# Optimization experiments

Hardware: AMD Instinct MI355X
Metric: run time of the kernel (lower is better)

Reference implementation:

```python
import jax, jax.numpy as jnp
import numpy as np

B, S, NE, E, H = 4, 2048, 8, 1024, 16
DH = E // H


def setup_inputs() -> dict:
    key = jax.random.key(0)
    ks = jax.random.split(key, 10)
    s = 0.02
    return {
        "x": jax.random.normal(ks[0], (B, S, E), dtype=jnp.float32),
        "w1": jax.random.normal(ks[1], (NE, 4 * E, E), dtype=jnp.float32) * s,
        "b1": jnp.zeros((NE, 4 * E), dtype=jnp.float32),
        "w2": jax.random.normal(ks[2], (NE, E, 4 * E), dtype=jnp.float32) * s,
        "b2": jnp.zeros((NE, E), dtype=jnp.float32),
        "in_proj_w": jax.random.normal(ks[3], (3 * E, E), dtype=jnp.float32) * s,
        "in_proj_b": jnp.zeros((3 * E,), dtype=jnp.float32),
        "out_w": jax.random.normal(ks[4], (E, E), dtype=jnp.float32) * s,
        "out_b": jnp.zeros((E,), dtype=jnp.float32),
        "expert_id": 3,
    }


def reference(x, w1, b1, w2, b2, in_proj_w, in_proj_b, out_w, out_b, expert_id):
    # Per-expert FFN: [B,S,E] -> [B,S,NE,E]
    h = jax.nn.relu(jnp.einsum("bse,nfe->bsnf", x, w1) + b1)
    eo = jnp.einsum("bsnf,nef->bsne", h, w2) + b2  # [B,S,NE,E]

    # Multihead self-attention over the expert axis, batched over (B,S).
    wq, wk, wv = in_proj_w[:E], in_proj_w[E:2 * E], in_proj_w[2 * E:]
    bq, bk, bv = in_proj_b[:E], in_proj_b[E:2 * E], in_proj_b[2 * E:]
    q = (eo @ wq.T + bq).reshape(B, S, NE, H, DH)
    k = (eo @ wk.T + bk).reshape(B, S, NE, H, DH)
    v = (eo @ wv.T + bv).reshape(B, S, NE, H, DH)

    scale = 1.0 / jnp.sqrt(jnp.asarray(DH, dtype=q.dtype))
    # torch additive float mask: tril of ONES added to logits (not -inf masking)
    add_mask = jnp.tril(jnp.ones((NE, NE), dtype=q.dtype))
    logits = jnp.einsum("bsqhd,bskhd->bshqk", q, k) * scale + add_mask
    attn = jax.nn.softmax(logits, axis=-1)
    o = jnp.einsum("bshqk,bskhd->bsqhd", attn, v).reshape(B, S, NE, E)
    o = o @ out_w.T + out_b  # [B,S,NE,E]

    return o[:, :, expert_id, :]  # [B,S,E]
```

## Files before the change

### kernel.cpp

```cpp
#include <hip/hip_runtime.h>

typedef __bf16 bf16x8 __attribute__((ext_vector_type(8)));
typedef float  f32x4  __attribute__((ext_vector_type(4)));

__device__ __forceinline__ float bf2f(unsigned short u) {
    union { unsigned int i; float f; } x; x.i = ((unsigned int)u) << 16; return x.f;
}
__device__ __forceinline__ unsigned short f2bf(float f) {
    union { float f; unsigned int i; } x; x.f = f;
    unsigned int r = x.i + 0x7fff + ((x.i >> 16) & 1);
    return (unsigned short)(r >> 16);
}

__device__ __forceinline__ void gload16(const void* g, void* l) {
    __builtin_amdgcn_global_load_lds(
        (const __attribute__((address_space(1))) void*)g,
        (__attribute__((address_space(3))) void*)l, 16, 0, 0);
}

__global__ __launch_bounds__(256) void cvt_f32_bf16(
    const float4* __restrict__ in, ushort4* __restrict__ out, long n4)
{
    long i = (long)blockIdx.x * blockDim.x + threadIdx.x;
    const long stride = (long)gridDim.x * blockDim.x;
    for (; i < n4; i += stride) {
        const float4 v = in[i];
        ushort4 o = { f2bf(v.x), f2bf(v.y), f2bf(v.z), f2bf(v.w) };
        out[i] = o;
    }
}

template<bool RELU, typename CT, bool QKV>
__global__ __launch_bounds__(512, 2) void gemm256(
    const ushort* __restrict__ A, long lda, long sAz,
    const ushort* __restrict__ B, long ldb, long sBz,
    const float* __restrict__ bias, long sBiasz,
    CT* __restrict__ C, long ldc, long sCz,
    ushort* __restrict__ qc, ushort* __restrict__ kvc,
    int K, const int* __restrict__ eid_p)
{
    const long z  = blockIdx.z;
    const int gx  = gridDim.x;
    const int nwg = gx * gridDim.y;
    int wg = blockIdx.y * gx + blockIdx.x;
    if ((nwg & 7) == 0) wg = (wg & 7) * (nwg >> 3) + (wg >> 3);
    const long n0 = (long)(wg % gx) * 256;
    const long m0 = (long)(wg / gx) * 256;

    if constexpr (QKV) {
        if (n0 < 1024 && z != (long)(*eid_p)) return;
    }
    A    += z * sAz;
    B    += z * sBz;
    bias += z * sBiasz;
    if constexpr (!QKV) C += z * sCz;

    __shared__ alignas(16) ushort As[4][256 * 32];
    __shared__ alignas(16) ushort Bs[4][256 * 32];

    const int t    = threadIdx.x;
    const int wid  = t >> 6;
    const int lane = t & 63;
    const int lr   = lane & 15;
    const int lq   = lane >> 4;
    const int wr   = wid >> 2;
    const int wc   = wid & 3;

    const int d0 = wid * 1024 + lane * 16;
    const int s0 = d0 ^ (((d0 >> 7) & 3) << 4);
    const int r0 = s0 >> 6;
    const int c0 = (s0 & 63) >> 1;
    const ushort* aG0 = A + (m0 + r0) * lda + c0;
    const ushort* aG1 = A + (m0 + r0 + 128) * lda + c0;
    const ushort* bG0 = B + (n0 + r0) * ldb + c0;
    const ushort* bG1 = B + (n0 + r0 + 128) * ldb + c0;
    const int ldsOff = wid * 512;

    const int chnk  = lq ^ ((lr >> 1) & 3);
    const int aBase = (wr * 128 + lr) * 32 + chnk * 8;
    const int bBase = (wc * 64  + lr) * 32 + chnk * 8;

    const int nt = K >> 5;

    #define STAGE(buf_, kt_) { \
        const long ko_ = (long)(kt_) * 32; \
        gload16(aG0 + ko_, (void*)&As[buf_][ldsOff]); \
        gload16(aG1 + ko_, (void*)&As[buf_][4096 + ldsOff]); \
        gload16(bG0 + ko_, (void*)&Bs[buf_][ldsOff]); \
        gload16(bG1 + ko_, (void*)&Bs[buf_][4096 + ldsOff]); }

    STAGE(0, 0)
    if (nt > 1) STAGE(1, 1)
    if (nt > 2) STAGE(2, 2)

    f32x4 acc[8][4];
#pragma unroll
    for (int i = 0; i < 8; i++)
#pragma unroll
        for (int j = 0; j < 4; j++) acc[i][j] = (f32x4){0.f, 0.f, 0.f, 0.f};

    for (int kt = 0; kt < nt; ++kt) {
        const int rem = nt - 1 - kt;
        if (rem >= 2)      asm volatile("s_waitcnt vmcnt(8)" ::: "memory");
        else if (rem == 1) asm volatile("s_waitcnt vmcnt(4)" ::: "memory");
        else               asm volatile("s_waitcnt vmcnt(0)" ::: "memory");
        __builtin_amdgcn_s_barrier();
        __builtin_amdgcn_sched_barrier(0);

        if (kt + 3 < nt) STAGE((kt + 3) & 3, kt + 3)

        const ushort* as_ = As[kt & 3];
        const ushort* bs_ = Bs[kt & 3];
        bf16x8 af[8], bfr[4];
#pragma unroll
        for (int i = 0; i < 8; i++) af[i]  = *(const bf16x8*)&as_[aBase + i * 512];
#pragma unroll
        for (int j = 0; j < 4; j++) bfr[j] = *(const bf16x8*)&bs_[bBase + j * 512];

        __builtin_amdgcn_s_setprio(1);
#pragma unroll
        for (int i = 0; i < 8; i++)
#pragma unroll
            for (int j = 0; j < 4; j++)
                acc[i][j] = __builtin_amdgcn_mfma_f32_16x16x32_bf16(af[i], bfr[j], acc[i][j], 0, 0, 0);
        __builtin_amdgcn_s_setprio(0);
    }
    #undef STAGE

#pragma unroll
    for (int j = 0; j < 4; j++) {
        const long col = n0 + wc * 64 + j * 16 + lr;
        const float bv = bias[col];
#pragma unroll
        for (int i = 0; i < 8; i++) {
            const long rbase = m0 + wr * 128 + i * 16 + lq * 4;
#pragma unroll
            for (int r = 0; r < 4; r++) {
                float v = acc[i][j][r] + bv;
                if (RELU) v = fmaxf(v, 0.f);
                const long row = rbase + r;
                if constexpr (QKV) {
                    if (col < 1024) qc[row * 1024 + col] = f2bf(v);
                    else            kvc[row * 16384 + z * 2048 + (col - 1024)] = f2bf(v);
                } else if constexpr (__is_same(CT, ushort)) {
                    C[row * ldc + col] = f2bf(v);
                } else {
                    C[row * ldc + col] = v;
                }
            }
        }
    }
}

__global__ __launch_bounds__(256) void attn_kernel(
    const ushort* __restrict__ qc, const ushort* __restrict__ kvc,
    const int* __restrict__ eid_p, ushort* __restrict__ o3)
{
    const size_t m = blockIdx.x;
    const int t    = threadIdx.x;
    const int h    = t >> 4;
    const int d0   = (t & 15) * 4;
    const int eid  = *eid_p;

    const ushort4 qu = *(const ushort4*)(qc + m * 1024 + h * 64 + d0);
    const float qv[4] = { bf2f(qu.x), bf2f(qu.y), bf2f(qu.z), bf2f(qu.w) };

    float l[8];
#pragma unroll
    for (int n = 0; n < 8; n++) {
        const ushort4 ku = *(const ushort4*)(kvc + (m * 8 + n) * 2048 + h * 64 + d0);
        float p = qv[0] * bf2f(ku.x) + qv[1] * bf2f(ku.y) + qv[2] * bf2f(ku.z) + qv[3] * bf2f(ku.w);
        p += __shfl_xor(p, 1);
        p += __shfl_xor(p, 2);
        p += __shfl_xor(p, 4);
        p += __shfl_xor(p, 8);
        l[n] = p * 0.125f + ((n <= eid) ? 1.0f : 0.0f);
    }
    float mx = l[0];
#pragma unroll
    for (int n = 1; n < 8; n++) mx = fmaxf(mx, l[n]);
    float e[8], s = 0.f;
#pragma unroll
    for (int n = 0; n < 8; n++) { e[n] = __expf(l[n] - mx); s += e[n]; }
    const float inv = 1.f / s;

    float o[4] = {0.f, 0.f, 0.f, 0.f};
#pragma unroll
    for (int n = 0; n < 8; n++) {
        const ushort4 vu = *(const ushort4*)(kvc + (m * 8 + n) * 2048 + 1024 + h * 64 + d0);
        const float a = e[n] * inv;
        o[0] += a * bf2f(vu.x); o[1] += a * bf2f(vu.y);
        o[2] += a * bf2f(vu.z); o[3] += a * bf2f(vu.w);
    }
    ushort4 ou = { f2bf(o[0]), f2bf(o[1]), f2bf(o[2]), f2bf(o[3]) };
    *(ushort4*)(o3 + m * 1024 + h * 64 + d0) = ou;
}

extern "C" void kernel_launch(void* const* d_in, const int* in_sizes, int n_in,
                              void* d_out, int out_size, void* d_ws, size_t ws_size,
                              hipStream_t stream)
{
    const float* x   = (const float*)d_in[0];
    const float* w1  = (const float*)d_in[1];
    const float* b1  = (const float*)d_in[2];
    const float* w2  = (const float*)d_in[3];
    const float* b2  = (const float*)d_in[4];
    const float* ipw = (const float*)d_in[5];
    const float* ipb = (const float*)d_in[6];
    const float* ow  = (const float*)d_in[7];
    const float* ob  = (const float*)d_in[8];
    const int*   eid = (const int*)d_in[9];

    char* ws = (char*)d_ws;
    size_t off = 0;
    auto alloc = [&](size_t bytes) { char* p = ws + off; off += (bytes + 255) & ~(size_t)255; return p; };
    ushort* w1b  = (ushort*)alloc(8LL * 4096 * 1024 * 2);
    ushort* w2b  = (ushort*)alloc(8LL * 1024 * 4096 * 2);
    ushort* ipwb = (ushort*)alloc(3LL * 1024 * 1024 * 2);
    ushort* owb  = (ushort*)alloc(1LL * 1024 * 1024 * 2);
    ushort* xb   = (ushort*)alloc(8192LL * 1024 * 2);
    ushort* o3b  = (ushort*)alloc(8192LL * 1024 * 2);
    const size_t fixed = off;

    long Mc = 2048;
    while (Mc > 256 && fixed + (size_t)Mc * 116736 + 2048 > ws_size) Mc >>= 1;
    ushort* hb  = (ushort*)alloc((size_t)Mc * 8 * 4096 * 2);
    ushort* eob = (ushort*)alloc((size_t)Mc * 8 * 1024 * 2);
    ushort* kvc = (ushort*)alloc((size_t)Mc * 8 * 2048 * 2);
    ushort* qc  = (ushort*)alloc((size_t)Mc * 1024 * 2);

    const dim3 blk(256);
    const dim3 blk5(512);
    const dim3 cgrid(2048);

    cvt_f32_bf16<<<cgrid, blk, 0, stream>>>((const float4*)w1,  (ushort4*)w1b,  8LL * 4096 * 1024 / 4);
    cvt_f32_bf16<<<cgrid, blk, 0, stream>>>((const float4*)w2,  (ushort4*)w2b,  8LL * 1024 * 4096 / 4);
    cvt_f32_bf16<<<cgrid, blk, 0, stream>>>((const float4*)ipw, (ushort4*)ipwb, 3LL * 1024 * 1024 / 4);
    cvt_f32_bf16<<<cgrid, blk, 0, stream>>>((const float4*)ow,  (ushort4*)owb,  1LL * 1024 * 1024 / 4);
    cvt_f32_bf16<<<cgrid, blk, 0, stream>>>((const float4*)x,   (ushort4*)xb,   8192LL * 1024 / 4);

    for (long m0 = 0; m0 < 8192; m0 += Mc) {
        const unsigned my = (unsigned)(Mc / 256);
        gemm256<true, ushort, false><<<dim3(16, my, 8), blk5, 0, stream>>>(
            xb + m0 * 1024, 1024, 0,
            w1b, 1024, 4096LL * 1024,
            b1, 4096,
            hb, 4096, (long)Mc * 4096,
            nullptr, nullptr, 1024, eid);
        gemm256<false, ushort, false><<<dim3(4, my, 8), blk5, 0, stream>>>(
            hb, 4096, (long)Mc * 4096,
            w2b, 4096, 1024LL * 4096,
            b2, 1024,
            eob, 1024, (long)Mc * 1024,
            nullptr, nullptr, 4096, eid);
        gemm256<false, ushort, true><<<dim3(12, my, 8), blk5, 0, stream>>>(
            eob, 1024, (long)Mc * 1024,
            ipwb, 1024, 0,
            ipb, 0,
            (ushort*)nullptr, 0, 0,
            qc, kvc, 1024, eid);
        attn_kernel<<<dim3((unsigned)Mc), blk, 0, stream>>>(
            qc, kvc, eid, o3b + m0 * 1024);
    }

    gemm256<false, float, false><<<dim3(4, 32, 1), blk5, 0, stream>>>(
        o3b, 1024, 0,
        owb, 1024, 0,
        ob, 0,
        (float*)d_out, 1024, 0,
        nullptr, nullptr, 1024, eid);
}
```

Before: 2.641 ms.

## Split GEMM k-loop into two barrier-separated MFMA phases with staggered A/B prefetch

Restructures the bf16 GEMM main loop so each k-tile is processed in two halves of four row fragments each. The global-to-LDS prefetch for A is issued in the first half and for B in the second, with barriers and waitcnts placed around each MFMA burst. The aim is to spread memory issue across the compute phases, interleave LDS reads with MFMA, and cut register use by holding four A fragments instead of eight. The cost is more barriers per iteration and reliance on hand-tuned vmcnt counts.

```diff
diff --git a/kernel.cpp b/kernel.cpp
--- a/kernel.cpp
+++ b/kernel.cpp
@@ -82,16 +82,18 @@
 
     const int nt = K >> 5;
 
-    #define STAGE(buf_, kt_) { \
-        const long ko_ = (long)(kt_) * 32; \
+    #define STAGE_A(buf_, kt_) { const long ko_ = (long)(kt_) * 32; \
         gload16(aG0 + ko_, (void*)&As[buf_][ldsOff]); \
-        gload16(aG1 + ko_, (void*)&As[buf_][4096 + ldsOff]); \
+        gload16(aG1 + ko_, (void*)&As[buf_][4096 + ldsOff]); }
+    #define STAGE_B(buf_, kt_) { const long ko_ = (long)(kt_) * 32; \
         gload16(bG0 + ko_, (void*)&Bs[buf_][ldsOff]); \
         gload16(bG1 + ko_, (void*)&Bs[buf_][4096 + ldsOff]); }
 
-    STAGE(0, 0)
-    if (nt > 1) STAGE(1, 1)
-    if (nt > 2) STAGE(2, 2)
+    STAGE_A(0, 0) STAGE_B(0, 0)
+    if (nt > 1) { STAGE_A(1, 1) STAGE_B(1, 1) }
+    if (nt > 2) { STAGE_A(2, 2) STAGE_B(2, 2) }
+    asm volatile("s_waitcnt vmcnt(8)" ::: "memory");
+    __builtin_amdgcn_s_barrier();
 
     f32x4 acc[8][4];
 #pragma unroll
@@ -100,32 +102,53 @@
         for (int j = 0; j < 4; j++) acc[i][j] = (f32x4){0.f, 0.f, 0.f, 0.f};
 
     for (int kt = 0; kt < nt; ++kt) {
-        const int rem = nt - 1 - kt;
-        if (rem >= 2)      asm volatile("s_waitcnt vmcnt(8)" ::: "memory");
-        else if (rem == 1) asm volatile("s_waitcnt vmcnt(4)" ::: "memory");
-        else               asm volatile("s_waitcnt vmcnt(0)" ::: "memory");
-        __builtin_amdgcn_s_barrier();
-        __builtin_amdgcn_sched_barrier(0);
-
-        if (kt + 3 < nt) STAGE((kt + 3) & 3, kt + 3)
-
-        const ushort* as_ = As[kt & 3];
-        const ushort* bs_ = Bs[kt & 3];
-        bf16x8 af[8], bfr[4];
-#pragma unroll
-        for (int i = 0; i < 8; i++) af[i]  = *(const bf16x8*)&as_[aBase + i * 512];
+        const int r = kt & 3;
+        const ushort* as_ = As[r];
+        const ushort* bs_ = Bs[r];
+        const bool pf = (kt + 3 < nt);
+
+        bf16x8 af[4], bfr[4];
+#pragma unroll
+        for (int i = 0; i < 4; i++) af[i]  = *(const bf16x8*)&as_[aBase + i * 512];
 #pragma unroll
         for (int j = 0; j < 4; j++) bfr[j] = *(const bf16x8*)&bs_[bBase + j * 512];
-
+        if (pf) STAGE_A((kt + 3) & 3, kt + 3)
+        __builtin_amdgcn_s_barrier();
+        asm volatile("s_waitcnt lgkmcnt(0)" ::: "memory");
+        __builtin_amdgcn_sched_barrier(0);
         __builtin_amdgcn_s_setprio(1);
 #pragma unroll
-        for (int i = 0; i < 8; i++)
+        for (int i = 0; i < 4; i++)
 #pragma unroll
             for (int j = 0; j < 4; j++)
                 acc[i][j] = __builtin_amdgcn_mfma_f32_16x16x32_bf16(af[i], bfr[j], acc[i][j], 0, 0, 0);
         __builtin_amdgcn_s_setprio(0);
-    }
-    #undef STAGE
+        __builtin_amdgcn_sched_barrier(0);
+        __builtin_amdgcn_s_barrier();
+
+#pragma unroll
+        for (int i = 0; i < 4; i++) af[i] = *(const bf16x8*)&as_[aBase + (4 + i) * 512];
+        if (pf) STAGE_B((kt + 3) & 3, kt + 3)
+        __builtin_amdgcn_s_barrier();
+        asm volatile("s_waitcnt lgkmcnt(0)" ::: "memory");
+        __builtin_amdgcn_sched_barrier(0);
+        __builtin_amdgcn_s_setprio(1);
+#pragma unroll
+        for (int i = 0; i < 4; i++)
+#pragma unroll
+            for (int j = 0; j < 4; j++)
+                acc[4 + i][j] = __builtin_amdgcn_mfma_f32_16x16x32_bf16(af[i], bfr[j], acc[4 + i][j], 0, 0, 0);
+        __builtin_amdgcn_s_setprio(0);
+        __builtin_amdgcn_sched_barrier(0);
+
+        const int rem = nt - 1 - kt;
+        if (rem >= 3)      asm volatile("s_waitcnt vmcnt(8)" ::: "memory");
+        else if (rem == 2) asm volatile("s_waitcnt vmcnt(4)" ::: "memory");
+        else if (rem == 1) asm volatile("s_waitcnt vmcnt(0)" ::: "memory");
+        __builtin_amdgcn_s_barrier();
+    }
+    #undef STAGE_A
+    #undef STAGE_B
 
 #pragma unroll
     for (int j = 0; j < 4; j++) {
```

New measurement: 2.326 ms. -11.9%, faster.
